# Performance work log

Measured on AMD Instinct MI355X. Metric: run time of the kernel, lower is better.

Reference implementation:

```python
import jax, jax.numpy as jnp
import numpy as np

B, SQ, SK, H, NH = 8, 1024, 1024, 512, 4
D = H // NH
MASK_FILL = -2.0 ** 32 + 1
LN_EPS = 1e-5


def setup_inputs() -> dict:
    key = jax.random.key(0)
    ks = jax.random.split(key, 9)
    memory = jax.random.normal(ks[0], (B, SK, H), dtype=jnp.float32)
    decoder_input = jax.random.normal(ks[1], (B, SQ, H), dtype=jnp.float32)
    mask = jax.random.randint(ks[2], (B, SQ, SK), 0, 2).astype(bool)
    query_mask = jax.random.randint(ks[3], (B, SQ), 0, 2).astype(jnp.float32)
    # Linear weights stored torch-style as (out_dim, in_dim), xavier-ish scale
    scale = 1.0 / np.sqrt(H)
    Wk = jax.random.uniform(ks[4], (H, H), jnp.float32, -scale, scale)
    Wv = jax.random.uniform(ks[5], (H, H), jnp.float32, -scale, scale)
    Wq = jax.random.uniform(ks[6], (H, H), jnp.float32, -scale, scale)
    gamma = jnp.ones((H,), jnp.float32)
    beta = jnp.zeros((H,), jnp.float32)
    return {"memory": memory, "decoder_input": decoder_input, "mask": mask,
            "query_mask": query_mask, "Wk": Wk, "Wv": Wv, "Wq": Wq,
            "gamma": gamma, "beta": beta}


def reference(memory, decoder_input, mask, query_mask, Wk, Wv, Wq, gamma, beta):
    # projections (torch Linear: y = x @ W.T), split into heads
    k = jnp.einsum('bsh,oh->bso', memory, Wk).reshape(B, SK, NH, D)
    v = jnp.einsum('bsh,oh->bso', memory, Wv).reshape(B, SK, NH, D)
    q = jnp.einsum('bsh,oh->bso', decoder_input, Wq).reshape(B, SQ, NH, D)
    # scaled dot-product scores: [h, B, Sq, Sk]
    scores = jnp.einsum('bqhd,bkhd->hbqk', q, k) / jnp.sqrt(jnp.float32(D))
    scores = jnp.where(mask[None], jnp.float32(MASK_FILL), scores)
    attn = jax.nn.softmax(scores, axis=-1)
    # post-softmax multiplicative query mask
    attn = attn * query_mask[None, :, :, None]
    out = jnp.einsum('hbqk,bkhd->bqhd', attn, v).reshape(B, SQ, H)
    # residual + LayerNorm
    x = out + decoder_input
    mu = jnp.mean(x, axis=-1, keepdims=True)
    var = jnp.mean((x - mu) ** 2, axis=-1, keepdims=True)
    result = (x - mu) * jax.lax.rsqrt(var + LN_EPS) * gamma + beta
    # attn returned in torch layout [h*B, Sq, Sk]
    return result, attn.reshape(NH * B, SQ, SK)
```

## Files before the change

kernel.cpp:

```cpp
#include <hip/hip_runtime.h>
#include <hip/hip_bf16.h>
#include <stdint.h>

#define NB 8
#define NSQ 1024
#define NSK 1024
#define NHID 512
#define NHEAD 4
#define NDH 128

typedef __attribute__((ext_vector_type(8))) short short8;
typedef __attribute__((ext_vector_type(4))) float f32x4;

__device__ __forceinline__ unsigned short f2b(float f) {
  unsigned int u = __builtin_bit_cast(unsigned int, f);
  u = u + 0x7FFFu + ((u >> 16) & 1u);
  return (unsigned short)(u >> 16);
}

__device__ __forceinline__ short8 pack8(float4 a, float4 b) {
  short8 o;
  o[0] = (short)f2b(a.x); o[1] = (short)f2b(a.y);
  o[2] = (short)f2b(a.z); o[3] = (short)f2b(a.w);
  o[4] = (short)f2b(b.x); o[5] = (short)f2b(b.y);
  o[6] = (short)f2b(b.z); o[7] = (short)f2b(b.w);
  return o;
}

__device__ __forceinline__ void gl2lds16(const unsigned short* g, unsigned short* l) {
  __builtin_amdgcn_global_load_lds(
      (const __attribute__((address_space(1))) void*)g,
      (__attribute__((address_space(3))) void*)l, 16, 0, 0);
}

__global__ __launch_bounds__(256) void cvt_blocked(
    const float* __restrict__ dec, const float* __restrict__ mem,
    const float* __restrict__ Wq, const float* __restrict__ Wk,
    const float* __restrict__ Wv, unsigned short* __restrict__ decB,
    unsigned short* __restrict__ memB, unsigned short* __restrict__ WqB,
    unsigned short* __restrict__ WkB, unsigned short* __restrict__ WvB) {
  const int bid = blockIdx.x, tid = threadIdx.x;
  const float* src;
  unsigned short* dst;
  int base_row;
  if (bid < 2048) { src = dec; dst = decB; base_row = bid * 4; }
  else if (bid < 4096) { src = mem; dst = memB; base_row = (bid - 2048) * 4; }
  else {
    int w = bid - 4096;
    int wi = w >> 7;
    src = (wi == 0) ? Wq : (wi == 1) ? Wk : Wv;
    dst = (wi == 0) ? WqB : (wi == 1) ? WkB : WvB;
    base_row = (w & 127) * 4;
  }
  const int row = base_row + (tid >> 6);
  const int kpos = (tid & 63) * 8;
  const float* s = src + (size_t)row * 512 + kpos;
  float4 a0 = *(const float4*)s;
  float4 a1 = *(const float4*)(s + 4);
  const int mt = row >> 7, kt = kpos >> 6, pr = row & 127, c = (kpos & 63) >> 3;
  *(short8*)&dst[(size_t)(mt * 8 + kt) * 8192 + pr * 64 + ((c ^ (pr & 7)) * 8)] =
      pack8(a0, a1);
}

__global__ void pack_mask(const int* __restrict__ m, unsigned int* __restrict__ mw) {
  int w = blockIdx.x * blockDim.x + threadIdx.x;
  const int* src = m + (size_t)w * 32;
  unsigned int bits = 0;
#pragma unroll
  for (int j = 0; j < 32; j += 4) {
    int4 v = *(const int4*)(src + j);
    bits |= (v.x ? 1u << j : 0u) | (v.y ? 1u << (j + 1) : 0u) |
            (v.z ? 1u << (j + 2) : 0u) | (v.w ? 1u << (j + 3) : 0u);
  }
  int row = w >> 5, wi = w & 31;
  mw[(size_t)row * 32 + ((wi & 3) * 8 + (wi >> 2))] = bits;
}

template <int TR>
__global__ __launch_bounds__(256) void proj_gemm(const unsigned short* __restrict__ A,
                                                 const unsigned short* __restrict__ W,
                                                 unsigned short* __restrict__ Cb) {
  __shared__ unsigned short tA[2][8192];
  __shared__ unsigned short tB[2][8192];
  const int tid = threadIdx.x, lane = tid & 63, wave = tid >> 6;
  const int mt = blockIdx.x, h = blockIdx.y;
  const int wm = (wave & 1) * 64, wn = (wave >> 1) * 64;
  const int r15 = lane & 15, hi = lane >> 4;

  auto stage = [&](int kt, int sel) {
#pragma unroll
    for (int i = 0; i < 4; ++i) {
      int ci = i * 4 + wave;
      gl2lds16(A + (size_t)(mt * 8 + kt) * 8192 + ci * 512 + lane * 8,
               &tA[sel][ci * 512 + lane * 8]);
      gl2lds16(W + (size_t)(h * 8 + kt) * 8192 + ci * 512 + lane * 8,
               &tB[sel][ci * 512 + lane * 8]);
    }
  };

  f32x4 acc[4][4];
  for (int i = 0; i < 4; ++i)
    for (int j = 0; j < 4; ++j) acc[i][j] = (f32x4){0.f, 0.f, 0.f, 0.f};

  stage(0, 0);
  __syncthreads();
  for (int kt = 0; kt < 8; ++kt) {
    const int sel = kt & 1;
    if (kt < 7) stage(kt + 1, sel ^ 1);
    __builtin_amdgcn_s_setprio(1);
#pragma unroll
    for (int kk = 0; kk < 2; ++kk) {
      short8 af[4], bf[4];
#pragma unroll
      for (int mi = 0; mi < 4; ++mi) {
        int row = wm + mi * 16 + r15;
        af[mi] = *(short8*)&tA[sel][row * 64 + (((kk * 4 + hi) ^ (row & 7)) * 8)];
      }
#pragma unroll
      for (int ni = 0; ni < 4; ++ni) {
        int row = wn + ni * 16 + r15;
        bf[ni] = *(short8*)&tB[sel][row * 64 + (((kk * 4 + hi) ^ (row & 7)) * 8)];
      }
#pragma unroll
      for (int mi = 0; mi < 4; ++mi)
#pragma unroll
        for (int ni = 0; ni < 4; ++ni)
          acc[mi][ni] = __builtin_amdgcn_mfma_f32_16x16x32_bf16(
              af[mi], bf[ni], acc[mi][ni], 0, 0, 0);
    }
    __builtin_amdgcn_s_setprio(0);
    __syncthreads();
  }

#pragma unroll
  for (int mi = 0; mi < 4; ++mi)
#pragma unroll
    for (int ni = 0; ni < 4; ++ni)
#pragma unroll
      for (int r = 0; r < 4; ++r) {
        int m = mt * 128 + wm + mi * 16 + hi * 4 + r;
        int d = wn + ni * 16 + r15;
        int bq = m >> 10, q = m & 1023, t = q >> 7, pr = q & 127;
        size_t pbase = (size_t)((bq * 4 + h) * 8 + t) * 16384;
        unsigned short v = f2b(acc[mi][ni][r]);
        if (!TR)
          Cb[pbase + pr * 128 + (((d >> 3) ^ (pr & 7)) * 8) + (d & 7)] = v;
        else
          Cb[pbase + d * 128 + (((pr >> 3) ^ (d & 7)) * 8) + (pr & 7)] = v;
      }
}

__global__ __launch_bounds__(512, 4) void attn_s_kernel(
    const unsigned short* __restrict__ Qb, const unsigned short* __restrict__ Kb,
    const unsigned int* __restrict__ maskp, const float* __restrict__ qmask,
    float* __restrict__ attn) {
  __shared__ unsigned short tQ[32 * 128];
  __shared__ unsigned short buf0[128 * 128];
  __shared__ unsigned short buf1[128 * 128];
  __shared__ float redsum[32][8];
  const int L = blockIdx.x;
  const int r_ = L & 7;
  const int j_ = L >> 3;
  const int qt = j_ & 31;
  const int hb = (j_ >> 5) * 8 + r_;
  const int h = hb >> 3, b = hb & 7;
  const int q0 = qt * 32;
  const int tid = threadIdx.x;
  const int lane = tid & 63, wave = tid >> 6;
  const int r15 = lane & 15, hi = lane >> 4;

  auto stageK = [&](int t, unsigned short* buf) {
    const unsigned short* p = Kb + (size_t)((b * 4 + h) * 8 + t) * 16384;
#pragma unroll
    for (int i = 0; i < 4; ++i) {
      int ci = i * 8 + wave;
      gl2lds16(p + ci * 512 + lane * 8, buf + ci * 512 + lane * 8);
    }
  };
  {
    const unsigned short* p =
        Qb + (size_t)((b * 4 + h) * 8 + (q0 >> 7)) * 16384 + (q0 & 127) * 128;
    gl2lds16(p + wave * 512 + lane * 8, tQ + wave * 512 + lane * 8);
  }
  stageK(0, buf0);
  __syncthreads();

  f32x4 acc[2][8];
#pragma unroll
  for (int g = 0; g < 2; ++g)
#pragma unroll
    for (int t = 0; t < 8; ++t) acc[g][t] = (f32x4){0.f, 0.f, 0.f, 0.f};

#pragma unroll
  for (int t = 0; t < 8; ++t) {
    if (t < 7) stageK(t + 1, (t & 1) ? buf0 : buf1);
    const unsigned short* kb = (t & 1) ? buf1 : buf0;
    __builtin_amdgcn_s_setprio(1);
#pragma unroll
    for (int ks = 0; ks < 4; ++ks) {
      const int sw = ((ks * 4 + hi) ^ (r15 & 7)) * 8;
      short8 bk = *(const short8*)&kb[(wave * 16 + r15) * 128 + sw];
#pragma unroll
      for (int g = 0; g < 2; ++g) {
        short8 aqv = *(const short8*)&tQ[(g * 16 + r15) * 128 + sw];
        acc[g][t] = __builtin_amdgcn_mfma_f32_16x16x32_bf16(aqv, bk, acc[g][t], 0, 0, 0);
      }
    }
    __builtin_amdgcn_s_setprio(0);
    __syncthreads();
  }

  const float isd = 0.08838834764831845f;
  const int sh = (wave & 1) * 16 + r15;
#pragma unroll
  for (int g = 0; g < 2; ++g)
#pragma unroll
    for (int r = 0; r < 4; ++r) {
      const unsigned int* mrow =
          maskp + ((size_t)(b * NSQ) + q0 + g * 16 + hi * 4 + r) * 32 + (wave >> 1) * 8;
      uint4 wa = *(const uint4*)mrow;
      uint4 wb = *(const uint4*)(mrow + 4);
      unsigned int mw8[8] = {wa.x, wa.y, wa.z, wa.w, wb.x, wb.y, wb.z, wb.w};
      float sm = 0.f;
#pragma unroll
      for (int t = 0; t < 8; ++t) {
        unsigned int bit = (mw8[t] >> sh) & 1u;
        float s = acc[g][t][r] * isd;
        float e = __expf(bit ? -4294967296.0f : s);
        acc[g][t][r] = e;
        sm += e;
      }
      sm += __shfl_xor(sm, 1);
      sm += __shfl_xor(sm, 2);
      sm += __shfl_xor(sm, 4);
      sm += __shfl_xor(sm, 8);
      if (r15 == 0) redsum[g * 16 + hi * 4 + r][wave] = sm;
    }
  __syncthreads();
#pragma unroll
  for (int g = 0; g < 2; ++g)
#pragma unroll
    for (int r = 0; r < 4; ++r) {
      float4 a = *(float4*)&redsum[g * 16 + hi * 4 + r][0];
      float4 c = *(float4*)&redsum[g * 16 + hi * 4 + r][4];
      float sum = (a.x + a.y + a.z + a.w) + (c.x + c.y + c.z + c.w);
      float scl = qmask[b * NSQ + q0 + g * 16 + hi * 4 + r] / sum;
#pragma unroll
      for (int t = 0; t < 8; ++t) acc[g][t][r] *= scl;
    }

#pragma unroll
  for (int g = 0; g < 2; ++g) {
    float* abase =
        attn + ((size_t)hb * NSQ + q0 + g * 16 + hi * 4) * NSK + wave * 16 + r15;
#pragma unroll
    for (int t = 0; t < 8; ++t)
#pragma unroll
      for (int r = 0; r < 4; ++r) abase[(r << 10) + t * 128] = acc[g][t][r];
  }
}

__global__ __launch_bounds__(256) void pv_gemm(const float* __restrict__ attn,
                                               const unsigned short* __restrict__ Vtb,
                                               float* __restrict__ outh) {
  __shared__ unsigned short tA[128 * 128];
  __shared__ unsigned short tB[128 * 128];
  const int L = blockIdx.x;
  const int r_ = L & 7, q_ = (L >> 3) & 7, s_ = L >> 6;
  const int hb = s_ * 8 + r_;
  const int h = hb >> 3, b = hb & 7;
  const int m0 = q_ * 128;
  const int tid = threadIdx.x;
  const int lane = tid & 63;
  const int wave = tid >> 6;
  const int wm = (wave & 1) * 64;
  const int wn = (wave >> 1) * 64;
  const int r15 = lane & 15, hi = lane >> 4;
  const float* Abase = attn + (size_t)hb * NSQ * NSK;

  f32x4 acc[4][4];
  for (int i = 0; i < 4; ++i)
    for (int j = 0; j < 4; ++j) acc[i][j] = (f32x4){0.f, 0.f, 0.f, 0.f};

  for (int kt = 0; kt < 8; ++kt) {
    {
      const unsigned short* p = Vtb + (size_t)((b * 4 + h) * 8 + kt) * 16384;
#pragma unroll
      for (int i = 0; i < 8; ++i) {
        int ci = i * 4 + wave;
        gl2lds16(p + ci * 512 + lane * 8, tB + ci * 512 + lane * 8);
      }
    }
#pragma unroll
    for (int it = 0; it < 8; ++it) {
      int idx = it * 256 + tid;
      int row = idx >> 4, c = idx & 15;
      const float* sa = Abase + (size_t)(m0 + row) * NSK + kt * 128 + c * 8;
      float4 a0 = *(const float4*)sa;
      float4 a1 = *(const float4*)(sa + 4);
      *(short8*)&tA[row * 128 + ((c ^ (row & 7)) * 8)] = pack8(a0, a1);
    }
    __syncthreads();
    __builtin_amdgcn_s_setprio(1);
#pragma unroll
    for (int ks = 0; ks < 4; ++ks) {
      short8 af[4], bf[4];
#pragma unroll
      for (int mi = 0; mi < 4; ++mi) {
        int row = wm + mi * 16 + r15;
        af[mi] = *(short8*)&tA[row * 128 + (((ks * 4 + hi) ^ (row & 7)) * 8)];
      }
#pragma unroll
      for (int ni = 0; ni < 4; ++ni) {
        int row = wn + ni * 16 + r15;
        bf[ni] = *(short8*)&tB[row * 128 + (((ks * 4 + hi) ^ (row & 7)) * 8)];
      }
#pragma unroll
      for (int mi = 0; mi < 4; ++mi)
#pragma unroll
        for (int ni = 0; ni < 4; ++ni)
          acc[mi][ni] = __builtin_amdgcn_mfma_f32_16x16x32_bf16(
              af[mi], bf[ni], acc[mi][ni], 0, 0, 0);
    }
    __builtin_amdgcn_s_setprio(0);
    __syncthreads();
  }
#pragma unroll
  for (int mi = 0; mi < 4; ++mi)
#pragma unroll
    for (int ni = 0; ni < 4; ++ni)
#pragma unroll
      for (int r = 0; r < 4; ++r) {
        int m = m0 + wm + mi * 16 + hi * 4 + r;
        int n = wn + ni * 16 + r15;
        outh[(size_t)(b * NSQ + m) * NHID + h * NDH + n] = acc[mi][ni][r];
      }
}

__global__ __launch_bounds__(256) void ln_kernel(const float* __restrict__ outh,
                                                 const float* __restrict__ dec,
                                                 const float* __restrict__ gamma,
                                                 const float* __restrict__ beta,
                                                 float* __restrict__ result) {
  const int tid = threadIdx.x;
  const int lane = tid & 63, wave = tid >> 6;
  const size_t row = (size_t)blockIdx.x * 4 + wave;
  const float* xr = outh + row * NHID;
  const float* dr = dec + row * NHID;
  float v[8];
  float s = 0.f;
  for (int j = 0; j < 2; ++j) {
    float4 a = *(const float4*)(xr + lane * 8 + j * 4);
    float4 d = *(const float4*)(dr + lane * 8 + j * 4);
    v[j * 4 + 0] = a.x + d.x; v[j * 4 + 1] = a.y + d.y;
    v[j * 4 + 2] = a.z + d.z; v[j * 4 + 3] = a.w + d.w;
  }
  for (int j = 0; j < 8; ++j) s += v[j];
  for (int off = 32; off > 0; off >>= 1) s += __shfl_xor(s, off);
  float mu = s * (1.f / 512.f);
  float s2 = 0.f;
  for (int j = 0; j < 8; ++j) {
    float d = v[j] - mu;
    s2 += d * d;
  }
  for (int off = 32; off > 0; off >>= 1) s2 += __shfl_xor(s2, off);
  float rstd = rsqrtf(s2 * (1.f / 512.f) + 1e-5f);
  float* out = result + row * NHID;
  for (int j = 0; j < 2; ++j) {
    float4 g = *(const float4*)(gamma + lane * 8 + j * 4);
    float4 bt = *(const float4*)(beta + lane * 8 + j * 4);
    float4 o;
    o.x = (v[j * 4 + 0] - mu) * rstd * g.x + bt.x;
    o.y = (v[j * 4 + 1] - mu) * rstd * g.y + bt.y;
    o.z = (v[j * 4 + 2] - mu) * rstd * g.z + bt.z;
    o.w = (v[j * 4 + 3] - mu) * rstd * g.w + bt.w;
    *(float4*)(out + lane * 8 + j * 4) = o;
  }
}

extern "C" void kernel_launch(void* const* d_in, const int* in_sizes, int n_in,
                              void* d_out, int out_size, void* d_ws, size_t ws_size,
                              hipStream_t stream) {
  const float* memory = (const float*)d_in[0];
  const float* dec = (const float*)d_in[1];
  const int* mask = (const int*)d_in[2];
  const float* qmask = (const float*)d_in[3];
  const float* Wk = (const float*)d_in[4];
  const float* Wv = (const float*)d_in[5];
  const float* Wq = (const float*)d_in[6];
  const float* gamma = (const float*)d_in[7];
  const float* beta = (const float*)d_in[8];

  char* ws = (char*)d_ws;
  unsigned short* decBb = (unsigned short*)(ws + 0);
  unsigned short* memBb = (unsigned short*)(ws + 8388608);
  float* outh = (float*)(ws + 0);
  unsigned short* WqBb = (unsigned short*)(ws + 16777216);
  unsigned short* WkBb = (unsigned short*)(ws + 17301504);
  unsigned short* WvBb = (unsigned short*)(ws + 17825792);
  unsigned short* Qb = (unsigned short*)(ws + 18350080);
  unsigned short* Kb = (unsigned short*)(ws + 26738688);
  unsigned short* Vtb = (unsigned short*)(ws + 35127296);
  unsigned int* maskw = (unsigned int*)(ws + 43515904);

  float* resultp = (float*)d_out;
  float* attnp = resultp + 4194304;

  cvt_blocked<<<dim3(4480), dim3(256), 0, stream>>>(dec, memory, Wq, Wk, Wv, decBb,
                                                    memBb, WqBb, WkBb, WvBb);
  pack_mask<<<dim3(1024), dim3(256), 0, stream>>>(mask, maskw);
  proj_gemm<0><<<dim3(64, 4), dim3(256), 0, stream>>>(decBb, WqBb, Qb);
  proj_gemm<0><<<dim3(64, 4), dim3(256), 0, stream>>>(memBb, WkBb, Kb);
  proj_gemm<1><<<dim3(64, 4), dim3(256), 0, stream>>>(memBb, WvBb, Vtb);

  attn_s_kernel<<<dim3(1024), dim3(512), 0, stream>>>(Qb, Kb, maskw, qmask, attnp);
  pv_gemm<<<dim3(256), dim3(256), 0, stream>>>(attnp, Vtb, outh);
  ln_kernel<<<dim3(2048), dim3(256), 0, stream>>>(outh, dec, gamma, beta, resultp);
}
```

Before: 127.5 us.

## Merge Q/K/V projections into one launch and halve PV GEMM tile rows

```diff
diff --git a/kernel.cpp b/kernel.cpp
--- a/kernel.cpp
+++ b/kernel.cpp
@@ -37,8 +37,7 @@
     const float* __restrict__ dec, const float* __restrict__ mem,
     const float* __restrict__ Wq, const float* __restrict__ Wk,
     const float* __restrict__ Wv, unsigned short* __restrict__ decB,
-    unsigned short* __restrict__ memB, unsigned short* __restrict__ WqB,
-    unsigned short* __restrict__ WkB, unsigned short* __restrict__ WvB) {
+    unsigned short* __restrict__ memB, unsigned short* __restrict__ WB) {
   const int bid = blockIdx.x, tid = threadIdx.x;
   const float* src;
   unsigned short* dst;
@@ -49,7 +48,7 @@
     int w = bid - 4096;
     int wi = w >> 7;
     src = (wi == 0) ? Wq : (wi == 1) ? Wk : Wv;
-    dst = (wi == 0) ? WqB : (wi == 1) ? WkB : WvB;
+    dst = WB + (size_t)wi * 262144;
     base_row = (w & 127) * 4;
   }
   const int row = base_row + (tid >> 6);
@@ -76,12 +75,16 @@
   mw[(size_t)row * 32 + ((wi & 3) * 8 + (wi >> 2))] = bits;
 }
 
-template <int TR>
-__global__ __launch_bounds__(256) void proj_gemm(const unsigned short* __restrict__ A,
-                                                 const unsigned short* __restrict__ W,
-                                                 unsigned short* __restrict__ Cb) {
+__global__ __launch_bounds__(256) void proj_gemm_all(
+    const unsigned short* __restrict__ decB, const unsigned short* __restrict__ memB,
+    const unsigned short* __restrict__ WB, unsigned short* __restrict__ Cb) {
   __shared__ unsigned short tA[2][8192];
   __shared__ unsigned short tB[2][8192];
+  const int z = blockIdx.z;
+  const unsigned short* A = (z == 0) ? decB : memB;
+  const unsigned short* W = WB + (size_t)z * 262144;
+  unsigned short* C = Cb + (size_t)z * 4194304;
+  const bool tr = (z == 2);
   const int tid = threadIdx.x, lane = tid & 63, wave = tid >> 6;
   const int mt = blockIdx.x, h = blockIdx.y;
   const int wm = (wave & 1) * 64, wn = (wave >> 1) * 64;
@@ -143,10 +146,10 @@
         int bq = m >> 10, q = m & 1023, t = q >> 7, pr = q & 127;
         size_t pbase = (size_t)((bq * 4 + h) * 8 + t) * 16384;
         unsigned short v = f2b(acc[mi][ni][r]);
-        if (!TR)
-          Cb[pbase + pr * 128 + (((d >> 3) ^ (pr & 7)) * 8) + (d & 7)] = v;
+        if (!tr)
+          C[pbase + pr * 128 + (((d >> 3) ^ (pr & 7)) * 8) + (d & 7)] = v;
         else
-          Cb[pbase + d * 128 + (((pr >> 3) ^ (d & 7)) * 8) + (pr & 7)] = v;
+          C[pbase + d * 128 + (((pr >> 3) ^ (d & 7)) * 8) + (pr & 7)] = v;
       }
 }
 
@@ -263,24 +266,23 @@
 __global__ __launch_bounds__(256) void pv_gemm(const float* __restrict__ attn,
                                                const unsigned short* __restrict__ Vtb,
                                                float* __restrict__ outh) {
-  __shared__ unsigned short tA[128 * 128];
+  __shared__ unsigned short tA[64 * 128];
   __shared__ unsigned short tB[128 * 128];
   const int L = blockIdx.x;
-  const int r_ = L & 7, q_ = (L >> 3) & 7, s_ = L >> 6;
+  const int r_ = L & 7, q_ = (L >> 3) & 15, s_ = L >> 7;
   const int hb = s_ * 8 + r_;
   const int h = hb >> 3, b = hb & 7;
-  const int m0 = q_ * 128;
+  const int m0 = q_ * 64;
   const int tid = threadIdx.x;
   const int lane = tid & 63;
   const int wave = tid >> 6;
-  const int wm = (wave & 1) * 64;
-  const int wn = (wave >> 1) * 64;
+  const int wn = wave * 32;
   const int r15 = lane & 15, hi = lane >> 4;
   const float* Abase = attn + (size_t)hb * NSQ * NSK;
 
-  f32x4 acc[4][4];
+  f32x4 acc[4][2];
   for (int i = 0; i < 4; ++i)
-    for (int j = 0; j < 4; ++j) acc[i][j] = (f32x4){0.f, 0.f, 0.f, 0.f};
+    for (int j = 0; j < 2; ++j) acc[i][j] = (f32x4){0.f, 0.f, 0.f, 0.f};
 
   for (int kt = 0; kt < 8; ++kt) {
     {
@@ -292,7 +294,7 @@
       }
     }
 #pragma unroll
-    for (int it = 0; it < 8; ++it) {
+    for (int it = 0; it < 4; ++it) {
       int idx = it * 256 + tid;
       int row = idx >> 4, c = idx & 15;
       const float* sa = Abase + (size_t)(m0 + row) * NSK + kt * 128 + c * 8;
@@ -304,21 +306,21 @@
     __builtin_amdgcn_s_setprio(1);
 #pragma unroll
     for (int ks = 0; ks < 4; ++ks) {
-      short8 af[4], bf[4];
+      short8 af[4], bf[2];
 #pragma unroll
       for (int mi = 0; mi < 4; ++mi) {
-        int row = wm + mi * 16 + r15;
+        int row = mi * 16 + r15;
         af[mi] = *(short8*)&tA[row * 128 + (((ks * 4 + hi) ^ (row & 7)) * 8)];
       }
 #pragma unroll
-      for (int ni = 0; ni < 4; ++ni) {
+      for (int ni = 0; ni < 2; ++ni) {
         int row = wn + ni * 16 + r15;
         bf[ni] = *(short8*)&tB[row * 128 + (((ks * 4 + hi) ^ (row & 7)) * 8)];
       }
 #pragma unroll
       for (int mi = 0; mi < 4; ++mi)
 #pragma unroll
-        for (int ni = 0; ni < 4; ++ni)
+        for (int ni = 0; ni < 2; ++ni)
           acc[mi][ni] = __builtin_amdgcn_mfma_f32_16x16x32_bf16(
               af[mi], bf[ni], acc[mi][ni], 0, 0, 0);
     }
@@ -328,10 +330,10 @@
 #pragma unroll
   for (int mi = 0; mi < 4; ++mi)
 #pragma unroll
-    for (int ni = 0; ni < 4; ++ni)
+    for (int ni = 0; ni < 2; ++ni)
 #pragma unroll
       for (int r = 0; r < 4; ++r) {
-        int m = m0 + wm + mi * 16 + hi * 4 + r;
+        int m = m0 + mi * 16 + hi * 4 + r;
         int n = wn + ni * 16 + r15;
         outh[(size_t)(b * NSQ + m) * NHID + h * NDH + n] = acc[mi][ni][r];
       }
@@ -395,25 +397,23 @@
   unsigned short* decBb = (unsigned short*)(ws + 0);
   unsigned short* memBb = (unsigned short*)(ws + 8388608);
   float* outh = (float*)(ws + 0);
-  unsigned short* WqBb = (unsigned short*)(ws + 16777216);
-  unsigned short* WkBb = (unsigned short*)(ws + 17301504);
-  unsigned short* WvBb = (unsigned short*)(ws + 17825792);
-  unsigned short* Qb = (unsigned short*)(ws + 18350080);
-  unsigned short* Kb = (unsigned short*)(ws + 26738688);
-  unsigned short* Vtb = (unsigned short*)(ws + 35127296);
+  unsigned short* WB = (unsigned short*)(ws + 16777216);
+  unsigned short* QKVb = (unsigned short*)(ws + 18350080);
   unsigned int* maskw = (unsigned int*)(ws + 43515904);
+
+  unsigned short* Qb = QKVb;
+  unsigned short* Kb = QKVb + 4194304;
+  unsigned short* Vtb = QKVb + 8388608;
 
   float* resultp = (float*)d_out;
   float* attnp = resultp + 4194304;
 
   cvt_blocked<<<dim3(4480), dim3(256), 0, stream>>>(dec, memory, Wq, Wk, Wv, decBb,
-                                                    memBb, WqBb, WkBb, WvBb);
+                                                    memBb, WB);
   pack_mask<<<dim3(1024), dim3(256), 0, stream>>>(mask, maskw);
-  proj_gemm<0><<<dim3(64, 4), dim3(256), 0, stream>>>(decBb, WqBb, Qb);
-  proj_gemm<0><<<dim3(64, 4), dim3(256), 0, stream>>>(memBb, WkBb, Kb);
-  proj_gemm<1><<<dim3(64, 4), dim3(256), 0, stream>>>(memBb, WvBb, Vtb);
+  proj_gemm_all<<<dim3(64, 4, 3), dim3(256), 0, stream>>>(decBb, memBb, WB, QKVb);
 
   attn_s_kernel<<<dim3(1024), dim3(512), 0, stream>>>(Qb, Kb, maskw, qmask, attnp);
-  pv_gemm<<<dim3(256), dim3(256), 0, stream>>>(attnp, Vtb, outh);
+  pv_gemm<<<dim3(512), dim3(256), 0, stream>>>(attnp, Vtb, outh);
   ln_kernel<<<dim3(2048), dim3(256), 0, stream>>>(outh, dec, gamma, beta, resultp);
 }
```

Result: faster. 117.7 us (-7.7%).
